# Performance work log

Measured on AMD Instinct MI355X. Metric: run time of the kernel, lower is better.

The kernel has to match this reference:

```python
import jax, jax.numpy as jnp
import numpy as np

C = 256
RED = 2
CR = C // RED
B, D, H, W = 1, 16, 32, 32


def setup_inputs() -> dict:
    key = jax.random.key(0)
    ks = jax.random.split(key, 9)
    def w(k, o, i):
        return jax.random.normal(k, (o, i), dtype=jnp.float32) * (2.0 / i) ** 0.5
    return {
        "x": jax.random.normal(ks[0], (B, C, D, H, W), dtype=jnp.float32),
        "Wq": w(ks[1], CR, C), "bq": jnp.zeros((CR,), jnp.float32),
        "Wk": w(ks[2], CR, C), "bk": jnp.zeros((CR,), jnp.float32),
        "Wv": w(ks[3], CR, C), "bv": jnp.zeros((CR,), jnp.float32),
        "Wo": w(ks[4], C, CR) * 0.02, "bo": jnp.zeros((C,), jnp.float32),
    }


def reference(x, Wq, bq, Wk, bk, Wv, bv, Wo, bo):
    b, c, d, h, w = x.shape
    n = d * h * w
    scale = 1.0 / (c ** 0.5)
    xf = x.reshape(b, c, n)                      # [B, C, N]
    # 1x1x1 convs == per-voxel channel GEMMs
    q = jnp.einsum('oc,bcn->bno', Wq, xf) + bq   # [B, N, Cr]
    k = jnp.einsum('oc,bcn->bon', Wk, xf) + bk[:, None]  # [B, Cr, N]
    v = jnp.einsum('oc,bcn->bno', Wv, xf) + bv   # [B, N, Cr]
    attn = jnp.einsum('bnc,bcm->bnm', q, k) * scale      # [B, N, N]
    attn = jax.nn.softmax(attn, axis=-1)
    o = jnp.einsum('bnm,bmc->bnc', attn, v)      # [B, N, Cr]
    out = jnp.einsum('oc,bnc->bon', Wo, o) + bo[:, None]  # [B, C, N]
    return x + out.reshape(b, c, d, h, w)
```

## Files before the change

kernel.cpp:

```cpp
#include <hip/hip_runtime.h>

#define NTOK 16384
#define CCH  256
#define DH   128

typedef float f32x4  __attribute__((ext_vector_type(4)));
typedef short bf16x8 __attribute__((ext_vector_type(8)));
typedef short bf16x4 __attribute__((ext_vector_type(4)));

__device__ __forceinline__ unsigned short f2bf(float f) {
    unsigned int u = __builtin_bit_cast(unsigned int, f);
    u += 0x7fffu + ((u >> 16) & 1u);
    return (unsigned short)(u >> 16);
}
__device__ __forceinline__ float bf2f(unsigned short h) {
    unsigned int u = ((unsigned int)h) << 16;
    return __builtin_bit_cast(float, u);
}
__device__ __forceinline__ unsigned short f2bf_fast(float f) {
    unsigned int u = __builtin_bit_cast(unsigned int, f);
    return (unsigned short)((u + 0x8000u) >> 16);
}
__device__ __forceinline__ void load_lds16(const unsigned short* g, unsigned short* l) {
    __builtin_amdgcn_global_load_lds(
        (const __attribute__((address_space(1))) unsigned int*)g,
        (__attribute__((address_space(3))) unsigned int*)l, 16, 0, 0);
}

__global__ __launch_bounds__(256) void prep_w(
    const float* __restrict__ Wq, const float* __restrict__ Wk,
    const float* __restrict__ Wv, const float* __restrict__ Wo,
    unsigned short* __restrict__ Wqkv_bf, unsigned short* __restrict__ Wo_bf)
{
    int idx4 = (blockIdx.x * 256 + threadIdx.x) * 4;
    if (idx4 < 98304) {
        int wch = idx4 >> 15;
        int off = idx4 & 32767;
        const float* W = (wch == 0) ? Wq : ((wch == 1) ? Wk : Wv);
        float4 v = *(const float4*)(W + off);
        bf16x4 pk = { (short)f2bf(v.x), (short)f2bf(v.y),
                      (short)f2bf(v.z), (short)f2bf(v.w) };
        *(bf16x4*)(Wqkv_bf + idx4) = pk;
    } else {
        int off = idx4 - 98304;
        float4 v = *(const float4*)(Wo + off);
        bf16x4 pk = { (short)f2bf(v.x), (short)f2bf(v.y),
                      (short)f2bf(v.z), (short)f2bf(v.w) };
        *(bf16x4*)(Wo_bf + off) = pk;
    }
}

__global__ __launch_bounds__(256) void qkv_fused(
    const float* __restrict__ x, const unsigned short* __restrict__ Wqkv_bf,
    const float* __restrict__ bq, const float* __restrict__ bk,
    const float* __restrict__ bv,
    unsigned short* __restrict__ Qb, unsigned short* __restrict__ Kb,
    unsigned short* __restrict__ Vb)
{
    __shared__ unsigned short lX[32 * 264];
    __shared__ unsigned short lW[3 * DH * 40];

    const int t    = threadIdx.x;
    const int wave = t >> 6, lane = t & 63, l16 = lane & 15, quad = lane >> 4;
    const int nt   = blockIdx.x;

#pragma unroll
    for (int pass = 0; pass < 8; ++pass) {
        int c  = pass * 32 + (t >> 3);
        int n4 = t & 7;
        float4 xv = *(const float4*)(x + c * NTOK + nt * 32 + n4 * 4);
        lX[(n4 * 4 + 0) * 264 + c] = f2bf(xv.x);
        lX[(n4 * 4 + 1) * 264 + c] = f2bf(xv.y);
        lX[(n4 * 4 + 2) * 264 + c] = f2bf(xv.z);
        lX[(n4 * 4 + 3) * 264 + c] = f2bf(xv.w);
    }

    f32x4 acc[3][2][2];
#pragma unroll
    for (int wch = 0; wch < 3; ++wch)
#pragma unroll
        for (int os = 0; os < 2; ++os)
#pragma unroll
            for (int ns = 0; ns < 2; ++ns) acc[wch][os][ns] = (f32x4){0, 0, 0, 0};

    for (int kc8 = 0; kc8 < 8; ++kc8) {
        __syncthreads();
#pragma unroll
        for (int wch = 0; wch < 3; ++wch) {
            const unsigned short* Wb = Wqkv_bf + wch * 32768;
#pragma unroll
            for (int p = 0; p < 2; ++p) {
                int s = p * 256 + t;
                int row = s >> 2, oct = s & 3;
                bf16x8 wv = *(const bf16x8*)(Wb + row * CCH + kc8 * 32 + oct * 8);
                *(bf16x8*)(&lW[wch * DH * 40 + row * 40 + oct * 8]) = wv;
            }
        }
        __syncthreads();

        bf16x8 bfr[2];
#pragma unroll
        for (int ns = 0; ns < 2; ++ns)
            bfr[ns] = *(const bf16x8*)(&lX[(ns * 16 + l16) * 264 + kc8 * 32 + quad * 8]);
#pragma unroll
        for (int wch = 0; wch < 3; ++wch)
#pragma unroll
            for (int os = 0; os < 2; ++os) {
                bf16x8 afr = *(const bf16x8*)(&lW[wch * DH * 40 + (wave * 32 + os * 16 + l16) * 40 + quad * 8]);
                acc[wch][os][0] = __builtin_amdgcn_mfma_f32_16x16x32_bf16(afr, bfr[0], acc[wch][os][0], 0, 0, 0);
                acc[wch][os][1] = __builtin_amdgcn_mfma_f32_16x16x32_bf16(afr, bfr[1], acc[wch][os][1], 0, 0, 0);
            }
    }

#pragma unroll
    for (int wch = 0; wch < 3; ++wch) {
        const float* bias = (wch == 0) ? bq : ((wch == 1) ? bk : bv);
        const float oscale = (wch == 0) ? 0.0625f * 1.44269504f : 1.0f;
#pragma unroll
        for (int os = 0; os < 2; ++os)
#pragma unroll
            for (int ns = 0; ns < 2; ++ns)
#pragma unroll
                for (int r = 0; r < 4; ++r) {
                    int o = wave * 32 + os * 16 + quad * 4 + r;
                    int n = nt * 32 + ns * 16 + l16;
                    float v = (acc[wch][os][ns][r] + bias[o]) * oscale;
                    if (wch == 2)       Vb[o * NTOK + n] = f2bf(v);
                    else if (wch == 0)  Qb[n * DH + o]   = f2bf(v);
                    else                Kb[n * DH + o]   = f2bf(v);
                }
    }
}

#define LPS 64

__global__ __launch_bounds__(256, 2) void flash_attn(
    const unsigned short* __restrict__ Qb, const unsigned short* __restrict__ Kb,
    const unsigned short* __restrict__ Vb,
    unsigned short* __restrict__ P0, unsigned short* __restrict__ P123,
    float* __restrict__ lbuf, int niter)
{
    __shared__ unsigned short lK[64 * DH];
    __shared__ unsigned short lV[DH * 64];
    __shared__ unsigned short lP[4 * 32 * LPS];

    const int t    = threadIdx.x;
    const int wave = t >> 6, lane = t & 63, l16 = lane & 15, quad = lane >> 4;
    const int qrow0 = blockIdx.x * 128 + wave * 32;
    const int split = blockIdx.y;
    const int tile0 = split * niter;
    const int xorP  = (l16 & 7) << 3;

    bf16x8 qa[2][4];
#pragma unroll
    for (int h = 0; h < 2; ++h)
#pragma unroll
        for (int kc = 0; kc < 4; ++kc)
            qa[h][kc] = *(const bf16x8*)(Qb + (qrow0 + h * 16 + l16) * DH + kc * 32 + quad * 8);

    f32x4 acc[2][8];
#pragma unroll
    for (int h = 0; h < 2; ++h)
#pragma unroll
        for (int i = 0; i < 8; ++i) acc[h][i] = (f32x4){0, 0, 0, 0};
    float lpart[2] = {0.f, 0.f};

    for (int it = 0; it < niter; ++it) {
        __syncthreads();
        {
            const unsigned short* Kt = Kb + (size_t)(tile0 + it) * 64 * DH;
            const int vcol = (tile0 + it) * 64;
#pragma unroll
            for (int p = 0; p < 4; ++p) {
                int s = p * 256 + t;
                int key = s >> 4, c16 = s & 15;
                load_lds16(Kt + key * DH + ((c16 ^ (key & 15)) << 3),
                           &lK[(p * 256 + wave * 64) * 8]);
                int vr = s >> 3, vc = s & 7;
                load_lds16(Vb + vr * NTOK + vcol + ((vc ^ (vr & 7)) << 3),
                           &lV[(p * 256 + wave * 64) * 8]);
            }
        }
        __syncthreads();

        f32x4 sf[2][4];
#pragma unroll
        for (int h = 0; h < 2; ++h)
#pragma unroll
            for (int ns = 0; ns < 4; ++ns) sf[h][ns] = (f32x4){0, 0, 0, 0};
        __builtin_amdgcn_s_setprio(1);
#pragma unroll
        for (int kc = 0; kc < 4; ++kc) {
#pragma unroll
            for (int ns = 0; ns < 4; ++ns) {
                bf16x8 kb = *(const bf16x8*)(&lK[(ns * 16 + l16) * DH + (((kc * 4 + quad) ^ l16) << 3)]);
                sf[0][ns] = __builtin_amdgcn_mfma_f32_16x16x32_bf16(kb, qa[0][kc], sf[0][ns], 0, 0, 0);
                sf[1][ns] = __builtin_amdgcn_mfma_f32_16x16x32_bf16(kb, qa[1][kc], sf[1][ns], 0, 0, 0);
            }
        }
        __builtin_amdgcn_s_setprio(0);

        unsigned short* pb = &lP[wave * 32 * LPS];
#pragma unroll
        for (int h = 0; h < 2; ++h)
#pragma unroll
            for (int ns = 0; ns < 4; ++ns) {
                float p0 = __builtin_amdgcn_exp2f(sf[h][ns][0]);
                float p1 = __builtin_amdgcn_exp2f(sf[h][ns][1]);
                float p2 = __builtin_amdgcn_exp2f(sf[h][ns][2]);
                float p3 = __builtin_amdgcn_exp2f(sf[h][ns][3]);
                lpart[h] += (p0 + p1) + (p2 + p3);
                bf16x4 pk = { (short)f2bf_fast(p0), (short)f2bf_fast(p1),
                              (short)f2bf_fast(p2), (short)f2bf_fast(p3) };
                *(bf16x4*)(pb + (h * 16 + l16) * LPS + ((ns * 16 + quad * 4) ^ xorP)) = pk;
            }

        bf16x8 pa[2][2];
#pragma unroll
        for (int h = 0; h < 2; ++h)
#pragma unroll
            for (int half = 0; half < 2; ++half)
                pa[h][half] = *(const bf16x8*)(pb + (h * 16 + l16) * LPS + ((half * 32 + quad * 8) ^ xorP));

        __builtin_amdgcn_s_setprio(1);
#pragma unroll
        for (int ds = 0; ds < 8; ++ds) {
            bf16x8 vb0 = *(const bf16x8*)(&lV[(ds * 16 + l16) * 64 + ((quad ^ (l16 & 7)) << 3)]);
            bf16x8 vb1 = *(const bf16x8*)(&lV[(ds * 16 + l16) * 64 + (((4 + quad) ^ (l16 & 7)) << 3)]);
            acc[0][ds] = __builtin_amdgcn_mfma_f32_16x16x32_bf16(pa[0][0], vb0, acc[0][ds], 0, 0, 0);
            acc[0][ds] = __builtin_amdgcn_mfma_f32_16x16x32_bf16(pa[0][1], vb1, acc[0][ds], 0, 0, 0);
            acc[1][ds] = __builtin_amdgcn_mfma_f32_16x16x32_bf16(pa[1][0], vb0, acc[1][ds], 0, 0, 0);
            acc[1][ds] = __builtin_amdgcn_mfma_f32_16x16x32_bf16(pa[1][1], vb1, acc[1][ds], 0, 0, 0);
        }
        __builtin_amdgcn_s_setprio(0);
    }

    float lsum[2];
#pragma unroll
    for (int h = 0; h < 2; ++h) {
        float s = lpart[h];
        s += __shfl_xor(s, 16);
        s += __shfl_xor(s, 32);
        lsum[h] = s;
    }

    unsigned short* base = (split == 0) ? P0 : (P123 + (size_t)(split - 1) * NTOK * DH);
#pragma unroll
    for (int h = 0; h < 2; ++h) {
        float inv[4];
#pragma unroll
        for (int r = 0; r < 4; ++r)
            inv[r] = 1.0f / __shfl(lsum[h], quad * 4 + r, 16);
#pragma unroll
        for (int ds = 0; ds < 8; ++ds)
#pragma unroll
            for (int r = 0; r < 4; ++r) {
                int row = qrow0 + h * 16 + quad * 4 + r;
                base[row * DH + ds * 16 + l16] = f2bf(acc[h][ds][r] * inv[r]);
            }
        if (quad == 0)
            lbuf[split * NTOK + qrow0 + h * 16 + l16] = lsum[h];
    }
}

template <int NS>
__global__ __launch_bounds__(256) void combine(
    const unsigned short* __restrict__ P123, const float* __restrict__ lbuf,
    unsigned short* __restrict__ Ob)
{
    const int t = threadIdx.x;
    const int n  = blockIdx.x * 32 + (t >> 3);
    const int sg = t & 7;

    const unsigned short* Pp[NS];
    Pp[0] = Ob;
#pragma unroll
    for (int s = 1; s < NS; ++s) Pp[s] = P123 + (size_t)(s - 1) * NTOK * DH;

    float w[NS], den = 0.f;
#pragma unroll
    for (int s = 0; s < NS; ++s) { w[s] = lbuf[s * NTOK + n]; den += w[s]; }
    float invden = 1.0f / den;
#pragma unroll
    for (int s = 0; s < NS; ++s) w[s] *= invden;

#pragma unroll
    for (int j = 0; j < 2; ++j) {
        bf16x8 v[NS];
#pragma unroll
        for (int s = 0; s < NS; ++s)
            v[s] = *(const bf16x8*)(Pp[s] + n * DH + sg * 16 + j * 8);
        bf16x8 o;
#pragma unroll
        for (int e = 0; e < 8; ++e) {
            float a = 0.f;
#pragma unroll
            for (int s = 0; s < NS; ++s)
                a += w[s] * bf2f((unsigned short)v[s][e]);
            o[e] = (short)f2bf(a);
        }
        *(bf16x8*)(Ob + n * DH + sg * 16 + j * 8) = o;
    }
}

__global__ __launch_bounds__(256) void out_proj(
    const unsigned short* __restrict__ Wo_bf, const float* __restrict__ bo,
    const float* __restrict__ x, const unsigned short* __restrict__ Ob,
    float* __restrict__ out)
{
    __shared__ unsigned short lW[DH * 72];
    __shared__ float lsO[DH * 68];

    const int t    = threadIdx.x;
    const int wave = t >> 6, lane = t & 63, l16 = lane & 15, quad = lane >> 4;
    const int ch = blockIdx.x & 1;
    const int n0 = (blockIdx.x >> 1) * 64;
    const int c0 = ch * 128;

#pragma unroll
    for (int i = 0; i < 8; ++i) {
        int s = i * 256 + t;
        int row = s >> 4, oct = s & 15;
        bf16x8 wv = *(const bf16x8*)(Wo_bf + (c0 + row) * DH + oct * 8);
        *(bf16x8*)(&lW[row * 72 + oct * 8]) = wv;
    }
    __syncthreads();

    f32x4 acc[8];
#pragma unroll
    for (int i = 0; i < 8; ++i) acc[i] = (f32x4){0, 0, 0, 0};

#pragma unroll
    for (int kc = 0; kc < 4; ++kc) {
        bf16x8 bfr = *(const bf16x8*)(Ob + (n0 + wave * 16 + l16) * DH + kc * 32 + quad * 8);
#pragma unroll
        for (int cs = 0; cs < 8; ++cs) {
            bf16x8 afr = *(const bf16x8*)(&lW[(cs * 16 + l16) * 72 + kc * 32 + quad * 8]);
            acc[cs] = __builtin_amdgcn_mfma_f32_16x16x32_bf16(afr, bfr, acc[cs], 0, 0, 0);
        }
    }

#pragma unroll
    for (int cs = 0; cs < 8; ++cs)
#pragma unroll
        for (int r = 0; r < 4; ++r)
            lsO[(cs * 16 + quad * 4 + r) * 68 + wave * 16 + l16] = acc[cs][r];
    __syncthreads();

#pragma unroll
    for (int it = 0; it < 8; ++it) {
        int idx = it * 256 + t;
        int c  = idx >> 4;
        int n4 = idx & 15;
        float4 v = *(const float4*)(&lsO[c * 68 + n4 * 4]);
        float4 xv = *(const float4*)(x + (size_t)(c0 + c) * NTOK + n0 + n4 * 4);
        float b = bo[c0 + c];
        float4 o = { v.x + b + xv.x, v.y + b + xv.y, v.z + b + xv.z, v.w + b + xv.w };
        *(float4*)(out + (size_t)(c0 + c) * NTOK + n0 + n4 * 4) = o;
    }
}

extern "C" void kernel_launch(void* const* d_in, const int* in_sizes, int n_in,
                              void* d_out, int out_size, void* d_ws, size_t ws_size,
                              hipStream_t stream) {
    const float* x  = (const float*)d_in[0];
    const float* Wq = (const float*)d_in[1];
    const float* bq = (const float*)d_in[2];
    const float* Wk = (const float*)d_in[3];
    const float* bk = (const float*)d_in[4];
    const float* Wv = (const float*)d_in[5];
    const float* bv = (const float*)d_in[6];
    const float* Wo = (const float*)d_in[7];
    const float* bo = (const float*)d_in[8];
    float* out = (float*)d_out;

    char* w = (char*)d_ws;
    unsigned short* Qb = (unsigned short*)(w);
    unsigned short* Kb = (unsigned short*)(w + (4u << 20));
    unsigned short* Vb = (unsigned short*)(w + (8u << 20));
    unsigned short* Ob = (unsigned short*)(w + (12u << 20));

    const size_t lbuf_off  = (44u << 20);
    const size_t wbf_offA  = lbuf_off + 8 * NTOK * sizeof(float);
    const size_t needA     = wbf_offA + (256u << 10);

    if (ws_size >= needA) {
        unsigned short* P123    = (unsigned short*)(w + (16u << 20));
        float*          lbuf    = (float*)(w + lbuf_off);
        unsigned short* Wqkv_bf = (unsigned short*)(w + wbf_offA);
        unsigned short* Wo_bf   = Wqkv_bf + 3 * DH * CCH;

        prep_w<<<128, 256, 0, stream>>>(Wq, Wk, Wv, Wo, Wqkv_bf, Wo_bf);
        qkv_fused<<<512, 256, 0, stream>>>(x, Wqkv_bf, bq, bk, bv, Qb, Kb, Vb);
        flash_attn<<<dim3(128, 8), 256, 0, stream>>>(Qb, Kb, Vb, Ob, P123, lbuf, 32);
        combine<8><<<512, 256, 0, stream>>>(P123, lbuf, Ob);
        out_proj<<<512, 256, 0, stream>>>(Wo_bf, bo, x, Ob, out);
    } else {
        unsigned short* P123    = (unsigned short*)d_out;
        float*          lbuf    = (float*)((char*)d_out + (12u << 20));
        unsigned short* Wqkv_bf = (unsigned short*)(w + (16u << 20));
        unsigned short* Wo_bf   = Wqkv_bf + 3 * DH * CCH;

        prep_w<<<128, 256, 0, stream>>>(Wq, Wk, Wv, Wo, Wqkv_bf, Wo_bf);
        qkv_fused<<<512, 256, 0, stream>>>(x, Wqkv_bf, bq, bk, bv, Qb, Kb, Vb);
        flash_attn<<<dim3(128, 4), 256, 0, stream>>>(Qb, Kb, Vb, Ob, P123, lbuf, 64);
        combine<4><<<512, 256, 0, stream>>>(P123, lbuf, Ob);
        out_proj<<<512, 256, 0, stream>>>(Wo_bf, bo, x, Ob, out);
    }
}
```

Measured before the change: 246.2 us.

## Stage QKV epilogue through LDS for coalesced stores and use 4-way key split

The QKV projection epilogue now packs results into LDS and writes Q, K and V to global memory as 16-byte vectors, replacing scattered 2-byte stores. Separately, the flash-attention launch drops from an 8-way to a 4-way key split in the large-workspace path, doubling iterations per block, and the workspace layout shrinks to match. Coalesced stores cut memory transactions in the projection kernel. The smaller split halves the partial outputs the combine kernel must merge, at the cost of fewer blocks and less parallelism in attention. The extra barriers and LDS round-trips add some latency.

```diff
diff --git a/kernel.cpp b/kernel.cpp
--- a/kernel.cpp
+++ b/kernel.cpp
@@ -3,6 +3,7 @@
 #define NTOK 16384
 #define CCH  256
 #define DH   128
+#define KSPLIT 4
 
 typedef float f32x4  __attribute__((ext_vector_type(4)));
 typedef short bf16x8 __attribute__((ext_vector_type(8)));
@@ -112,23 +113,53 @@
             }
     }
 
-#pragma unroll
-    for (int wch = 0; wch < 3; ++wch) {
-        const float* bias = (wch == 0) ? bq : ((wch == 1) ? bk : bv);
+    unsigned short* lE = lX;
+
+#pragma unroll
+    for (int wch = 0; wch < 2; ++wch) {
+        const float* bias = (wch == 0) ? bq : bk;
         const float oscale = (wch == 0) ? 0.0625f * 1.44269504f : 1.0f;
+        __syncthreads();
 #pragma unroll
         for (int os = 0; os < 2; ++os)
 #pragma unroll
-            for (int ns = 0; ns < 2; ++ns)
-#pragma unroll
-                for (int r = 0; r < 4; ++r) {
-                    int o = wave * 32 + os * 16 + quad * 4 + r;
-                    int n = nt * 32 + ns * 16 + l16;
-                    float v = (acc[wch][os][ns][r] + bias[o]) * oscale;
-                    if (wch == 2)       Vb[o * NTOK + n] = f2bf(v);
-                    else if (wch == 0)  Qb[n * DH + o]   = f2bf(v);
-                    else                Kb[n * DH + o]   = f2bf(v);
-                }
+            for (int ns = 0; ns < 2; ++ns) {
+                int o0 = wave * 32 + os * 16 + quad * 4;
+                bf16x4 pk;
+#pragma unroll
+                for (int r = 0; r < 4; ++r)
+                    pk[r] = (short)f2bf((acc[wch][os][ns][r] + bias[o0 + r]) * oscale);
+                *(bf16x4*)(&lE[(ns * 16 + l16) * 136 + o0]) = pk;
+            }
+        __syncthreads();
+        unsigned short* dst = (wch == 0) ? Qb : Kb;
+#pragma unroll
+        for (int it = 0; it < 2; ++it) {
+            int idx = it * 256 + t;
+            int n = idx >> 4, o8 = idx & 15;
+            *(bf16x8*)(dst + (size_t)(nt * 32 + n) * DH + o8 * 8) =
+                *(const bf16x8*)(&lE[n * 136 + o8 * 8]);
+        }
+    }
+
+    __syncthreads();
+#pragma unroll
+    for (int os = 0; os < 2; ++os)
+#pragma unroll
+        for (int ns = 0; ns < 2; ++ns)
+#pragma unroll
+            for (int r = 0; r < 4; ++r) {
+                int o = wave * 32 + os * 16 + quad * 4 + r;
+                int n = ns * 16 + l16;
+                lE[o * 40 + n] = f2bf(acc[2][os][ns][r] + bv[o]);
+            }
+    __syncthreads();
+#pragma unroll
+    for (int it = 0; it < 2; ++it) {
+        int idx = it * 256 + t;
+        int o = idx >> 2, f = idx & 3;
+        *(bf16x8*)(Vb + (size_t)o * NTOK + nt * 32 + f * 8) =
+            *(const bf16x8*)(&lE[o * 40 + f * 8]);
     }
 }
 
@@ -380,8 +411,8 @@
     unsigned short* Vb = (unsigned short*)(w + (8u << 20));
     unsigned short* Ob = (unsigned short*)(w + (12u << 20));
 
-    const size_t lbuf_off  = (44u << 20);
-    const size_t wbf_offA  = lbuf_off + 8 * NTOK * sizeof(float);
+    const size_t lbuf_off  = (28u << 20);
+    const size_t wbf_offA  = lbuf_off + KSPLIT * NTOK * sizeof(float);
     const size_t needA     = wbf_offA + (256u << 10);
 
     if (ws_size >= needA) {
@@ -392,8 +423,8 @@
 
         prep_w<<<128, 256, 0, stream>>>(Wq, Wk, Wv, Wo, Wqkv_bf, Wo_bf);
         qkv_fused<<<512, 256, 0, stream>>>(x, Wqkv_bf, bq, bk, bv, Qb, Kb, Vb);
-        flash_attn<<<dim3(128, 8), 256, 0, stream>>>(Qb, Kb, Vb, Ob, P123, lbuf, 32);
-        combine<8><<<512, 256, 0, stream>>>(P123, lbuf, Ob);
+        flash_attn<<<dim3(128, KSPLIT), 256, 0, stream>>>(Qb, Kb, Vb, Ob, P123, lbuf, 64);
+        combine<KSPLIT><<<512, 256, 0, stream>>>(P123, lbuf, Ob);
         out_proj<<<512, 256, 0, stream>>>(Wo_bf, bo, x, Ob, out);
     } else {
         unsigned short* P123    = (unsigned short*)d_out;
@@ -403,8 +434,8 @@
 
         prep_w<<<128, 256, 0, stream>>>(Wq, Wk, Wv, Wo, Wqkv_bf, Wo_bf);
         qkv_fused<<<512, 256, 0, stream>>>(x, Wqkv_bf, bq, bk, bv, Qb, Kb, Vb);
-        flash_attn<<<dim3(128, 4), 256, 0, stream>>>(Qb, Kb, Vb, Ob, P123, lbuf, 64);
-        combine<4><<<512, 256, 0, stream>>>(P123, lbuf, Ob);
+        flash_attn<<<dim3(128, KSPLIT), 256, 0, stream>>>(Qb, Kb, Vb, Ob, P123, lbuf, 64);
+        combine<KSPLIT><<<512, 256, 0, stream>>>(P123, lbuf, Ob);
         out_proj<<<512, 256, 0, stream>>>(Wo_bf, bo, x, Ob, out);
     }
 }
```

Result: no change. 243.8 us (-1.0%).
